# Kernel optimization log

Hardware: AMD Instinct MI355X
Metric: run time of the kernel (lower is better)

The kernel has to match this reference:

```python
import jax, jax.numpy as jnp
import numpy as np

D = 16      # core_size
R = 8       # rank
SIZE = D ** 3  # 4096, nr_cores = 3


def setup_inputs() -> dict:
    key = jax.random.key(0)
    k = jax.random.split(key, 5)
    core_std = np.sqrt(2.0 / D).astype(np.float32)  # kaiming_normal over (-1, d, d)
    x = jax.random.normal(k[0], (8, 1024, SIZE), dtype=jnp.float32)
    core0 = core_std * jax.random.normal(k[1], (D, D, D, D, R, 1), dtype=jnp.float32)
    core1 = core_std * jax.random.normal(k[2], (D, D, D, D, R, R), dtype=jnp.float32)
    core2 = core_std * jax.random.normal(k[3], (D, D, D, D, 1, R), dtype=jnp.float32)
    bias = np.sqrt(1.0 / SIZE).astype(np.float32) * jax.random.uniform(
        k[4], (SIZE,), dtype=jnp.float32, minval=-1.0, maxval=1.0)
    return {"x": x, "core0": core0, "core1": core1, "core2": core2, "bias": bias}


def to_matrix(core0, core1, core2):
    # Faithful translation of BTT.to_matrix for nr_cores=3.
    # G starts as core0: (d,d,d,d,r,1)
    # step idx=0 (core1): j=d, i=d^2
    c1 = core1.reshape(D, D * D, D, R, R)          # jixcb
    g = core0.reshape(D, D * D, D, R, 1)           # jiyba
    G = jnp.einsum('jixcb,jiyba->jiyxca', c1, g)   # (d, d^2, d, d, r, 1)
    # step idx=1 (core2): j=d^2, i=d
    c2 = core2.reshape(D * D, D, D, 1, R)          # jixcb
    g = G.reshape(D * D, D, D * D, R, 1)           # jiyba
    G = jnp.einsum('jixcb,jiyba->jiyxca', c2, g)   # (d^2, d, d^2, d, 1, 1)
    return G.reshape(SIZE, SIZE)


def reference(x, core0, core1, core2, bias):
    G = to_matrix(core0, core1, core2)
    out = x.reshape(-1, SIZE) @ G + bias
    return out.reshape(x.shape)
```

## Files before the change

### kernel.cpp

```cpp
#include <hip/hip_runtime.h>
#include <stdint.h>

typedef unsigned short u16;
typedef short bf16x8 __attribute__((ext_vector_type(8)));
typedef float f32x4 __attribute__((ext_vector_type(4)));
typedef u16 u16x4 __attribute__((ext_vector_type(4)));

__device__ __forceinline__ u16 f2bf(float f) {
    union { float f; unsigned int i; } v; v.f = f;
    unsigned int x = v.i;
    return (u16)((x + 0x7FFFu + ((x >> 16) & 1u)) >> 16);
}

__device__ __forceinline__ void async_load16(const u16* g, u16* lds) {
    __builtin_amdgcn_global_load_lds(
        (const __attribute__((address_space(1))) unsigned int*)g,
        (__attribute__((address_space(3))) unsigned int*)lds,
        16, 0, 0);
}

__global__ void transpose_f32(const float* __restrict__ in, float* __restrict__ out,
                              int Q) {
    __shared__ float t[64][65];
    const int r0 = blockIdx.y * 64;
    const int q0 = blockIdx.x * 64;
    const int tx = threadIdx.x & 63;
    const int ty = threadIdx.x >> 6;
    #pragma unroll
    for (int k = 0; k < 16; ++k) {
        const int row = k * 4 + ty;
        t[row][tx] = in[(size_t)(r0 + row) * Q + q0 + tx];
    }
    __syncthreads();
    #pragma unroll
    for (int k = 0; k < 16; ++k) {
        const int qrow = k * 4 + ty;
        out[(size_t)(q0 + qrow) * 4096 + r0 + tx] = t[tx][qrow];
    }
}

__global__ void build_gt_t(const float* __restrict__ c0t, const float* __restrict__ c1t,
                           const float* __restrict__ c2t, u16* __restrict__ Gt) {
    const int y1 = blockIdx.x >> 4;
    const int x1 = blockIdx.x & 15;
    const int r0 = blockIdx.y * 1024 + threadIdx.x * 4;

    f32x4 a0[8];
    #pragma unroll
    for (int b = 0; b < 8; ++b)
        a0[b] = *(const f32x4*)(c0t + (size_t)(y1 * 8 + b) * 4096 + r0);

    f32x4 t[8];
    #pragma unroll
    for (int c = 0; c < 8; ++c) {
        f32x4 s = {0.f, 0.f, 0.f, 0.f};
        #pragma unroll
        for (int b = 0; b < 8; ++b) {
            f32x4 w = *(const f32x4*)(c1t + (size_t)(x1 * 64 + c * 8 + b) * 4096 + r0);
            s += w * a0[b];
        }
        t[c] = s;
    }
    #pragma unroll
    for (int x2 = 0; x2 < 16; ++x2) {
        f32x4 s = {0.f, 0.f, 0.f, 0.f};
        #pragma unroll
        for (int c = 0; c < 8; ++c) {
            f32x4 w = *(const f32x4*)(c2t + (size_t)(x2 * 8 + c) * 4096 + r0);
            s += w * t[c];
        }
        u16x4 o;
        #pragma unroll
        for (int j = 0; j < 4; ++j) o[j] = f2bf(s[j]);
        *(u16x4*)(Gt + (size_t)(blockIdx.x * 16 + x2) * 4096 + r0) = o;
    }
}

__global__ void build_gt(const float* __restrict__ c0, const float* __restrict__ c1,
                         const float* __restrict__ c2, u16* __restrict__ Gt) {
    const int y1  = blockIdx.x >> 4;
    const int x1  = blockIdx.x & 15;
    const int r   = blockIdx.y * 256 + threadIdx.x;

    float a0[8];
    {
        f32x4 v0 = *(const f32x4*)(c0 + ((size_t)r * 16 + y1) * 8);
        f32x4 v1 = *(const f32x4*)(c0 + ((size_t)r * 16 + y1) * 8 + 4);
        #pragma unroll
        for (int b = 0; b < 4; ++b) { a0[b] = v0[b]; a0[4 + b] = v1[b]; }
    }
    float t[8];
    const float* c1row = c1 + ((size_t)r * 16 + x1) * 64;
    #pragma unroll
    for (int c = 0; c < 8; ++c) {
        f32x4 v0 = *(const f32x4*)(c1row + c * 8);
        f32x4 v1 = *(const f32x4*)(c1row + c * 8 + 4);
        float s = 0.f;
        #pragma unroll
        for (int b = 0; b < 4; ++b) s += v0[b] * a0[b] + v1[b] * a0[4 + b];
        t[c] = s;
    }
    const float* c2row = c2 + (size_t)r * 128;
    #pragma unroll
    for (int x2 = 0; x2 < 16; ++x2) {
        f32x4 v0 = *(const f32x4*)(c2row + x2 * 8);
        f32x4 v1 = *(const f32x4*)(c2row + x2 * 8 + 4);
        float s = 0.f;
        #pragma unroll
        for (int c = 0; c < 4; ++c) s += v0[c] * t[c] + v1[c] * t[4 + c];
        Gt[((size_t)(blockIdx.x * 16 + x2)) * 4096 + r] = f2bf(s);
    }
}

__global__ void conv_x(const f32x4* __restrict__ x, u16* __restrict__ xb, int n4) {
    for (int i = blockIdx.x * 256 + threadIdx.x; i < n4; i += gridDim.x * 256) {
        f32x4 v = x[i];
        u16x4 o;
        #pragma unroll
        for (int j = 0; j < 4; ++j) o[j] = f2bf(v[j]);
        *(u16x4*)(xb + 4 * (size_t)i) = o;
    }
}

__global__ __launch_bounds__(512, 2)
void gemm_8ph(const u16* __restrict__ Xb, const u16* __restrict__ Gt,
              const float* __restrict__ bias, float* __restrict__ out) {
    constexpr int K = 4096, N = 4096, NT = 64;
    extern __shared__ u16 lds[];

    const int tid  = threadIdx.x;
    const int lane = tid & 63;
    const int w    = tid >> 6;
    const int wmi  = w >> 2;
    const int wni  = w & 3;
    const int lr   = lane & 15;
    const int lq   = lane >> 4;
    const int xr   = lr & 7;

    const int m0 = blockIdx.y * 256;
    const int n0 = blockIdx.x * 256;

    const int r0 = tid >> 3;
    const int s0 = (tid & 7) ^ (r0 & 7);
    const int r1 = 64 + r0;
    const int s1 = ((512 + tid) & 7) ^ (r1 & 7);
    const size_t aoff0 = (size_t)(m0 + r0) * K + s0 * 8;
    const size_t aoff1 = (size_t)(m0 + r1) * K + s1 * 8;
    const size_t boff0 = (size_t)(n0 + r0) * K + s0 * 8;
    const size_t boff1 = (size_t)(n0 + r1) * K + s1 * 8;
    const int ldsw0 = (tid & ~63) * 8;
    const int ldsw1 = 4096 + (tid & ~63) * 8;

    const int aoffL = (wmi * 16 + lr) * 64;
    const int boffL = 16384 + (wni * 16 + lr) * 64;
    const int slot0 = (lq ^ xr) * 8;
    const int slot1 = ((4 + lq) ^ xr) * 8;

    f32x4 acc[8][4] = {};
    bf16x8 a[4][2];
    bf16x8 bfr[2][2][2];

    auto stageA = [&](int bb, int h, int t) {
        const u16* s = Xb + (size_t)h * (128 * K) + (size_t)t * 64;
        u16* d = lds + bb * 32768 + h * 8192;
        async_load16(s + aoff0, d + ldsw0);
        async_load16(s + aoff1, d + ldsw1);
    };
    auto stageB = [&](int bb, int h, int t) {
        const u16* s = Gt + (size_t)h * (128 * K) + (size_t)t * 64;
        u16* d = lds + bb * 32768 + 16384 + h * 8192;
        async_load16(s + boff0, d + ldsw0);
        async_load16(s + boff1, d + ldsw1);
    };
    auto loadA = [&](int bb, int h) {
        const u16* p = lds + bb * 32768 + h * 8192 + aoffL;
        #pragma unroll
        for (int li = 0; li < 4; ++li) {
            a[li][0] = *(const bf16x8*)(p + li * 2048 + slot0);
            a[li][1] = *(const bf16x8*)(p + li * 2048 + slot1);
        }
    };
    auto loadB = [&](int bb, int h) {
        const u16* p = lds + bb * 32768 + h * 8192 + boffL;
        #pragma unroll
        for (int lj = 0; lj < 2; ++lj) {
            bfr[h][lj][0] = *(const bf16x8*)(p + lj * 4096 + slot0);
            bfr[h][lj][1] = *(const bf16x8*)(p + lj * 4096 + slot1);
        }
    };
    auto mfmaQ = [&](int mh, int nh) {
        #pragma unroll
        for (int li = 0; li < 4; ++li)
            #pragma unroll
            for (int lj = 0; lj < 2; ++lj) {
                f32x4 c = acc[mh * 4 + li][nh * 2 + lj];
                c = __builtin_amdgcn_mfma_f32_16x16x32_bf16(a[li][0], bfr[nh][lj][0], c, 0, 0, 0);
                c = __builtin_amdgcn_mfma_f32_16x16x32_bf16(a[li][1], bfr[nh][lj][1], c, 0, 0, 0);
                acc[mh * 4 + li][nh * 2 + lj] = c;
            }
    };

    stageA(0, 0, 0); stageB(0, 0, 0);
    stageA(0, 1, 0); stageB(0, 1, 0);
    stageA(1, 0, 1); stageB(1, 0, 1);
    asm volatile("s_waitcnt vmcnt(8)" ::: "memory");
    __builtin_amdgcn_s_barrier();

    for (int T = 0; T < NT; ++T) {
        const int bc = T & 1, bn = bc ^ 1;
        const int t1 = (T + 1) & (NT - 1);
        const int t2 = (T + 2) & (NT - 1);

        loadA(bc, 0); loadB(bc, 0);
        stageA(bn, 1, t1);
        __builtin_amdgcn_s_barrier();
        asm volatile("s_waitcnt lgkmcnt(0)" ::: "memory");
        __builtin_amdgcn_s_setprio(1);
        mfmaQ(0, 0);
        __builtin_amdgcn_s_setprio(0);
        asm volatile("s_waitcnt vmcnt(6)" ::: "memory");
        __builtin_amdgcn_s_barrier();

        loadB(bc, 1);
        stageB(bn, 1, t1);
        __builtin_amdgcn_s_barrier();
        asm volatile("s_waitcnt lgkmcnt(0)" ::: "memory");
        __builtin_amdgcn_s_setprio(1);
        mfmaQ(0, 1);
        __builtin_amdgcn_s_setprio(0);
        __builtin_amdgcn_s_barrier();

        loadA(bc, 1);
        stageA(bc, 0, t2);
        __builtin_amdgcn_s_barrier();
        asm volatile("s_waitcnt lgkmcnt(0)" ::: "memory");
        __builtin_amdgcn_s_setprio(1);
        mfmaQ(1, 0);
        __builtin_amdgcn_s_setprio(0);
        __builtin_amdgcn_s_barrier();

        stageB(bc, 0, t2);
        __builtin_amdgcn_s_barrier();
        __builtin_amdgcn_s_setprio(1);
        mfmaQ(1, 1);
        __builtin_amdgcn_s_setprio(0);
        asm volatile("s_waitcnt vmcnt(8)" ::: "memory");
        __builtin_amdgcn_s_barrier();
    }
    asm volatile("s_waitcnt vmcnt(0)" ::: "memory");

    #pragma unroll
    for (int j = 0; j < 4; ++j) {
        const int n = n0 + (j * 4 + wni) * 16 + lr;
        const float bv = bias[n];
        #pragma unroll
        for (int i = 0; i < 8; ++i) {
            const int mb = m0 + (2 * i + wmi) * 16 + lq * 4;
            #pragma unroll
            for (int r = 0; r < 4; ++r)
                out[(size_t)(mb + r) * N + n] = acc[i][j][r] + bv;
        }
    }
}

#define TM 128
#define TN 128
#define BK 32

__global__ void gemm_bt_f32(const float* __restrict__ Xf, const u16* __restrict__ Gt,
                            const float* __restrict__ bias, float* __restrict__ out) {
    constexpr int K = 4096, N = 4096;
    __shared__ __attribute__((aligned(16))) u16 As[TM * BK];
    __shared__ __attribute__((aligned(16))) u16 Bs[TN * BK];

    const int tid  = threadIdx.x;
    const int lane = tid & 63;
    const int w    = tid >> 6;
    const int m0   = blockIdx.y * TM;
    const int n0   = blockIdx.x * TN;
    const int wm   = (w >> 1) * 64;
    const int wn   = (w & 1) * 64;
    const int lr   = lane & 15;
    const int lk   = (lane >> 4) * 8;

    f32x4 acc[4][4] = {};

    const int srow   = tid >> 2;
    const int schunk = (tid & 3) * 8;
    const u16* grow0 = Gt + (size_t)(n0 + srow) * K + schunk;
    const u16* grow1 = Gt + (size_t)(n0 + 64 + srow) * K + schunk;
    u16* ldsB0 = &Bs[(tid & ~63) * 8];
    u16* ldsB1 = &Bs[(256 + (tid & ~63)) * 8];

    const float* xsrc = Xf + (size_t)(m0 + (tid >> 1)) * K + (tid & 1) * 16;
    u16* adst = &As[(tid >> 1) * BK + (tid & 1) * 16];

    for (int k0 = 0; k0 < K; k0 += BK) {
        __syncthreads();
        {
            f32x4 v0 = ((const f32x4*)(xsrc + k0))[0];
            f32x4 v1 = ((const f32x4*)(xsrc + k0))[1];
            f32x4 v2 = ((const f32x4*)(xsrc + k0))[2];
            f32x4 v3 = ((const f32x4*)(xsrc + k0))[3];
            bf16x8 w0, w1;
            #pragma unroll
            for (int j = 0; j < 4; ++j) {
                w0[j]     = (short)f2bf(v0[j]);
                w0[4 + j] = (short)f2bf(v1[j]);
                w1[j]     = (short)f2bf(v2[j]);
                w1[4 + j] = (short)f2bf(v3[j]);
            }
            *(bf16x8*)adst = w0;
            *(bf16x8*)(adst + 8) = w1;
        }
        async_load16(grow0 + k0, ldsB0);
        async_load16(grow1 + k0, ldsB1);
        __syncthreads();

        bf16x8 af[4], bg[4];
        #pragma unroll
        for (int i = 0; i < 4; ++i) {
            af[i] = *(const bf16x8*)(&As[(wm + i * 16 + lr) * BK + lk]);
            bg[i] = *(const bf16x8*)(&Bs[(wn + i * 16 + lr) * BK + lk]);
        }
        #pragma unroll
        for (int mt = 0; mt < 4; ++mt)
            #pragma unroll
            for (int nt = 0; nt < 4; ++nt)
                acc[mt][nt] = __builtin_amdgcn_mfma_f32_16x16x32_bf16(
                    af[mt], bg[nt], acc[mt][nt], 0, 0, 0);
    }

    #pragma unroll
    for (int nt = 0; nt < 4; ++nt) {
        const int n = n0 + wn + nt * 16 + lr;
        const float bv = bias[n];
        #pragma unroll
        for (int mt = 0; mt < 4; ++mt) {
            const int mbase = m0 + wm + mt * 16 + (lane >> 4) * 4;
            #pragma unroll
            for (int r = 0; r < 4; ++r) {
                out[(size_t)(mbase + r) * N + n] = acc[mt][nt][r] + bv;
            }
        }
    }
}

extern "C" void kernel_launch(void* const* d_in, const int* in_sizes, int n_in,
                              void* d_out, int out_size, void* d_ws, size_t ws_size,
                              hipStream_t stream) {
    const float* x    = (const float*)d_in[0];
    const float* c0   = (const float*)d_in[1];
    const float* c1   = (const float*)d_in[2];
    const float* c2   = (const float*)d_in[3];
    const float* bias = (const float*)d_in[4];
    float* out = (float*)d_out;

    const size_t GT_BYTES = (size_t)4096 * 4096 * sizeof(u16);
    const size_t XB_BYTES = (size_t)8192 * 4096 * sizeof(u16);
    u16* Gt = (u16*)d_ws;

    if (ws_size >= GT_BYTES + XB_BYTES) {
        char* scratch = (char*)d_ws + GT_BYTES;
        float* c1t = (float*)scratch;
        float* c0t = (float*)(scratch + (size_t)16 * 1024 * 1024);
        float* c2t = (float*)(scratch + (size_t)18 * 1024 * 1024);

        transpose_f32<<<dim3(16, 64), 256, 0, stream>>>(c1, c1t, 1024);
        transpose_f32<<<dim3(2, 64), 256, 0, stream>>>(c0, c0t, 128);
        transpose_f32<<<dim3(2, 64), 256, 0, stream>>>(c2, c2t, 128);
        build_gt_t<<<dim3(256, 4), 256, 0, stream>>>(c0t, c1t, c2t, Gt);

        u16* Xb = (u16*)((char*)d_ws + GT_BYTES);
        conv_x<<<8192, 256, 0, stream>>>((const f32x4*)x, Xb, 8192 * 4096 / 4);

        static int attr_done = 0;
        if (!attr_done) {
            hipFuncSetAttribute(reinterpret_cast<const void*>(gemm_8ph),
                                hipFuncAttributeMaxDynamicSharedMemorySize, 131072);
            attr_done = 1;
        }
        gemm_8ph<<<dim3(16, 32), 512, 131072, stream>>>(Xb, Gt, bias, out);
    } else {
        build_gt<<<dim3(256, 16), 256, 0, stream>>>(c0, c1, c2, Gt);
        gemm_bt_f32<<<dim3(32, 64), 256, 0, stream>>>(x, Gt, bias, out);
    }
}
```

Before: 501.5 us.

## Restructure GEMM main loop pipeline and remap blocks for XCD locality

Result: no change. 498.7 us (-0.6%).

```diff
diff --git a/kernel.cpp b/kernel.cpp
--- a/kernel.cpp
+++ b/kernel.cpp
@@ -41,9 +41,13 @@
 
 __global__ void build_gt_t(const float* __restrict__ c0t, const float* __restrict__ c1t,
                            const float* __restrict__ c2t, u16* __restrict__ Gt) {
-    const int y1 = blockIdx.x >> 4;
-    const int x1 = blockIdx.x & 15;
-    const int r0 = blockIdx.y * 1024 + threadIdx.x * 4;
+    int id = blockIdx.x;
+    id = (id & 7) * 128 + (id >> 3);
+    const int x1 = id >> 6;
+    const int y1 = (id >> 2) & 15;
+    const int p  = id & 3;
+    const int r0 = p * 1024 + threadIdx.x * 4;
+    const int colb = (y1 * 16 + x1) * 16;
 
     f32x4 a0[8];
     #pragma unroll
@@ -72,7 +76,7 @@
         u16x4 o;
         #pragma unroll
         for (int j = 0; j < 4; ++j) o[j] = f2bf(s[j]);
-        *(u16x4*)(Gt + (size_t)(blockIdx.x * 16 + x2) * 4096 + r0) = o;
+        *(u16x4*)(Gt + (size_t)(colb + x2) * 4096 + r0) = o;
     }
 }
 
@@ -137,8 +141,10 @@
     const int lq   = lane >> 4;
     const int xr   = lr & 7;
 
-    const int m0 = blockIdx.y * 256;
-    const int n0 = blockIdx.x * 256;
+    int id = blockIdx.y * 16 + blockIdx.x;
+    id = (id & 7) * 64 + (id >> 3);
+    const int m0 = (id & 31) * 256;
+    const int n0 = (id >> 5) * 256;
 
     const int r0 = tid >> 3;
     const int s0 = (tid & 7) ^ (r0 & 7);
@@ -199,55 +205,61 @@
                 acc[mh * 4 + li][nh * 2 + lj] = c;
             }
     };
-
-    stageA(0, 0, 0); stageB(0, 0, 0);
-    stageA(0, 1, 0); stageB(0, 1, 0);
-    stageA(1, 0, 1); stageB(1, 0, 1);
+    auto mfmaQ_refillA = [&](int mh, int nh, const u16* pA) {
+        #pragma unroll
+        for (int li = 0; li < 4; ++li) {
+            #pragma unroll
+            for (int lj = 0; lj < 2; ++lj) {
+                f32x4 c = acc[mh * 4 + li][nh * 2 + lj];
+                c = __builtin_amdgcn_mfma_f32_16x16x32_bf16(a[li][0], bfr[nh][lj][0], c, 0, 0, 0);
+                c = __builtin_amdgcn_mfma_f32_16x16x32_bf16(a[li][1], bfr[nh][lj][1], c, 0, 0, 0);
+                acc[mh * 4 + li][nh * 2 + lj] = c;
+            }
+            a[li][0] = *(const bf16x8*)(pA + li * 2048 + slot0);
+            a[li][1] = *(const bf16x8*)(pA + li * 2048 + slot1);
+        }
+    };
+
+    stageA(0, 0, 0); stageB(0, 0, 0); stageA(0, 1, 0); stageB(0, 1, 0);
+    stageA(1, 0, 1); stageB(1, 0, 1); stageA(1, 1, 1); stageB(1, 1, 1);
     asm volatile("s_waitcnt vmcnt(8)" ::: "memory");
     __builtin_amdgcn_s_barrier();
+    loadB(0, 1); loadA(0, 0); loadB(0, 0);
 
     for (int T = 0; T < NT; ++T) {
         const int bc = T & 1, bn = bc ^ 1;
-        const int t1 = (T + 1) & (NT - 1);
         const int t2 = (T + 2) & (NT - 1);
 
-        loadA(bc, 0); loadB(bc, 0);
-        stageA(bn, 1, t1);
+        asm volatile("s_waitcnt lgkmcnt(0)" ::: "memory");
         __builtin_amdgcn_s_barrier();
-        asm volatile("s_waitcnt lgkmcnt(0)" ::: "memory");
+        __builtin_amdgcn_sched_barrier(0);
         __builtin_amdgcn_s_setprio(1);
         mfmaQ(0, 0);
         __builtin_amdgcn_s_setprio(0);
-        asm volatile("s_waitcnt vmcnt(6)" ::: "memory");
+
+        stageA(bc, 0, t2); stageB(bc, 0, t2);
+        __builtin_amdgcn_s_setprio(1);
+        mfmaQ_refillA(0, 1, lds + bc * 32768 + 8192 + aoffL);
+        __builtin_amdgcn_s_setprio(0);
+
+        asm volatile("s_waitcnt lgkmcnt(0)" ::: "memory");
         __builtin_amdgcn_s_barrier();
-
-        loadB(bc, 1);
-        stageB(bn, 1, t1);
-        __builtin_amdgcn_s_barrier();
-        asm volatile("s_waitcnt lgkmcnt(0)" ::: "memory");
-        __builtin_amdgcn_s_setprio(1);
-        mfmaQ(0, 1);
-        __builtin_amdgcn_s_setprio(0);
-        __builtin_amdgcn_s_barrier();
-
-        loadA(bc, 1);
-        stageA(bc, 0, t2);
-        __builtin_amdgcn_s_barrier();
-        asm volatile("s_waitcnt lgkmcnt(0)" ::: "memory");
-        __builtin_amdgcn_s_setprio(1);
-        mfmaQ(1, 0);
-        __builtin_amdgcn_s_setprio(0);
-        __builtin_amdgcn_s_barrier();
-
-        stageB(bc, 0, t2);
-        __builtin_amdgcn_s_barrier();
+        __builtin_amdgcn_sched_barrier(0);
         __builtin_amdgcn_s_setprio(1);
         mfmaQ(1, 1);
         __builtin_amdgcn_s_setprio(0);
+
+        stageA(bc, 1, t2); stageB(bc, 1, t2);
         asm volatile("s_waitcnt vmcnt(8)" ::: "memory");
         __builtin_amdgcn_s_barrier();
-    }
-    asm volatile("s_waitcnt vmcnt(0)" ::: "memory");
+        __builtin_amdgcn_sched_barrier(0);
+        loadB(bn, 1);
+        __builtin_amdgcn_s_setprio(1);
+        mfmaQ_refillA(1, 0, lds + bn * 32768 + aoffL);
+        __builtin_amdgcn_s_setprio(0);
+        loadB(bn, 0);
+    }
+    asm volatile("s_waitcnt vmcnt(0) lgkmcnt(0)" ::: "memory");
 
     #pragma unroll
     for (int j = 0; j < 4; ++j) {
@@ -369,7 +381,7 @@
         transpose_f32<<<dim3(16, 64), 256, 0, stream>>>(c1, c1t, 1024);
         transpose_f32<<<dim3(2, 64), 256, 0, stream>>>(c0, c0t, 128);
         transpose_f32<<<dim3(2, 64), 256, 0, stream>>>(c2, c2t, 128);
-        build_gt_t<<<dim3(256, 4), 256, 0, stream>>>(c0t, c1t, c2t, Gt);
+        build_gt_t<<<1024, 256, 0, stream>>>(c0t, c1t, c2t, Gt);
 
         u16* Xb = (u16*)((char*)d_ws + GT_BYTES);
         conv_x<<<8192, 256, 0, stream>>>((const f32x4*)x, Xb, 8192 * 4096 / 4);
```
